# Optimization experiments

Measured on AMD Instinct MI355X. Metric: run time of the kernel, lower is better.

The kernel has to match this reference:

```python
import jax, jax.numpy as jnp
import numpy as np

B, R, H, W = 8, 128, 4096, 4096

def setup_inputs() -> dict:
    key = jax.random.key(0)
    k1, k2, k3, k4 = jax.random.split(key, 4)
    N = jax.random.normal(k1, (B, 1, R, W), dtype=jnp.float32)
    Ak_L = jax.random.normal(k2, (B, 1, H, W), dtype=jnp.float32)
    alpha = jax.random.uniform(k3, (B,), dtype=jnp.float32)
    gamma = jax.random.uniform(k4, (B,), dtype=jnp.float32)
    return {"N": N, "Ak_L": Ak_L, "alpha": alpha, "gamma": gamma}

def reference(N, Ak_L, alpha, gamma):
    # N: [B,1,r,W], Ak_L: [B,1,H,W], alpha/gamma: [B]
    b = N.shape[0]
    r = N.shape[2]
    a = alpha.reshape(b, 1, 1, 1)
    g = gamma.reshape(b, 1, 1, 1)
    I = jnp.eye(r, dtype=N.dtype)  # broadcast over [B,1,r,r]
    # C = alpha*I + 2*gamma * N @ N^T  -> [B,1,r,r]
    C = a * I + 2.0 * g * jnp.einsum('bcrw,bcsw->bcrs', N, N)
    Cinv = jnp.linalg.pinv(C)  # batched pinv over [B,1]
    # X = (Ak_L @ N^T) @ pinv(C) -> [B,1,H,r]
    AN = jnp.einsum('bchw,bcrw->bchr', Ak_L, N)
    X = jnp.einsum('bchr,bcrs->bchs', AN, Cinv)
    return 2.0 * g * X
```

## Files before the change

### kernel.cpp

```cpp
#include <hip/hip_runtime.h>


typedef __attribute__((ext_vector_type(8))) short bf16x8;
typedef __attribute__((ext_vector_type(4))) float f32x4;
typedef __attribute__((ext_vector_type(4))) unsigned int u32x4;

#define MFMA16(a, b, c) __builtin_amdgcn_mfma_f32_16x16x32_bf16((a), (b), (c), 0, 0, 0)

__device__ __forceinline__ unsigned short f2bf(float f) {
  union { float f; unsigned u; } v; v.f = f;
  unsigned u = v.u;
  return (unsigned short)((u + 0x7FFFu + ((u >> 16) & 1u)) >> 16);
}
__device__ __forceinline__ unsigned pack2(float x, float y) {
  return (unsigned)f2bf(x) | ((unsigned)f2bf(y) << 16);
}

__global__ __launch_bounds__(256) void k_castT(const float* __restrict__ N,
                                               unsigned short* __restrict__ NT) {
  __attribute__((aligned(16))) __shared__ float tile[128 * 68];
  int wc = blockIdx.x, b = blockIdx.y;
  const float* Nb = N + (size_t)b * 524288 + wc * 64;
  int t = threadIdx.x;
  int row = t >> 1, half = t & 1;
  const float* src = Nb + (size_t)row * 4096 + half * 32;
  float* dst = tile + row * 68 + half * 32;
#pragma unroll
  for (int j = 0; j < 8; j++) *(f32x4*)(dst + j * 4) = *(const f32x4*)(src + j * 4);
  __syncthreads();
  int ow = t >> 2, q = t & 3;
  unsigned short* out = NT + (size_t)b * 524288 + (size_t)(wc * 64 + ow) * 128 + q * 32;
#pragma unroll
  for (int c = 0; c < 4; c++) {
    u32x4 p;
#pragma unroll
    for (int k = 0; k < 4; k++) {
      float f0 = tile[(q * 32 + c * 8 + k * 2) * 68 + ow];
      float f1 = tile[(q * 32 + c * 8 + k * 2 + 1) * 68 + ow];
      p[k] = pack2(f0, f1);
    }
    *(u32x4*)(out + c * 8) = p;
  }
}

__global__ __launch_bounds__(256) void k_gram(const float* __restrict__ N,
                                              float* __restrict__ Gpart) {
  __attribute__((aligned(16))) __shared__ unsigned short lds[128 * 72];
  int ks = blockIdx.x, b = blockIdx.y;
  const float* Nb = N + (size_t)b * 524288 + ks * 1024;
  int t = threadIdx.x;
  int wave = t >> 6, lane = t & 63, quad = lane >> 4, l16 = lane & 15;
  f32x4 acc[2][8];
#pragma unroll
  for (int i = 0; i < 2; i++)
#pragma unroll
    for (int j = 0; j < 8; j++) acc[i][j] = (f32x4){0.f, 0.f, 0.f, 0.f};
  int srow = t >> 1, shalf = t & 1;
  const float* srcb = Nb + (size_t)srow * 4096 + shalf * 32;
  unsigned short* dptr = lds + srow * 72 + shalf * 32;
  for (int it = 0; it < 16; ++it) {
    u32x4 pk0, pk1;
    {
      f32x4 v0 = *(const f32x4*)(srcb + it * 64 + 0);
      f32x4 v1 = *(const f32x4*)(srcb + it * 64 + 4);
      f32x4 v2 = *(const f32x4*)(srcb + it * 64 + 8);
      f32x4 v3 = *(const f32x4*)(srcb + it * 64 + 12);
      pk0[0] = pack2(v0[0], v0[1]); pk0[1] = pack2(v0[2], v0[3]);
      pk0[2] = pack2(v1[0], v1[1]); pk0[3] = pack2(v1[2], v1[3]);
      pk1[0] = pack2(v2[0], v2[1]); pk1[1] = pack2(v2[2], v2[3]);
      pk1[2] = pack2(v3[0], v3[1]); pk1[3] = pack2(v3[2], v3[3]);
    }
    u32x4 pk2, pk3;
    {
      f32x4 v0 = *(const f32x4*)(srcb + it * 64 + 16);
      f32x4 v1 = *(const f32x4*)(srcb + it * 64 + 20);
      f32x4 v2 = *(const f32x4*)(srcb + it * 64 + 24);
      f32x4 v3 = *(const f32x4*)(srcb + it * 64 + 28);
      pk2[0] = pack2(v0[0], v0[1]); pk2[1] = pack2(v0[2], v0[3]);
      pk2[2] = pack2(v1[0], v1[1]); pk2[3] = pack2(v1[2], v1[3]);
      pk3[0] = pack2(v2[0], v2[1]); pk3[1] = pack2(v2[2], v2[3]);
      pk3[2] = pack2(v3[0], v3[1]); pk3[3] = pack2(v3[2], v3[3]);
    }
    __syncthreads();
    *(u32x4*)(dptr + 0) = pk0;
    *(u32x4*)(dptr + 8) = pk1;
    *(u32x4*)(dptr + 16) = pk2;
    *(u32x4*)(dptr + 24) = pk3;
    __syncthreads();
    bf16x8 af[2][2], bfv[8][2];
#pragma unroll
    for (int mt = 0; mt < 2; mt++)
#pragma unroll
      for (int kk = 0; kk < 2; kk++)
        af[mt][kk] = *(const bf16x8*)(lds + (wave * 32 + mt * 16 + l16) * 72 + (kk * 4 + quad) * 8);
#pragma unroll
    for (int nt = 0; nt < 8; nt++)
#pragma unroll
      for (int kk = 0; kk < 2; kk++)
        bfv[nt][kk] = *(const bf16x8*)(lds + (nt * 16 + l16) * 72 + (kk * 4 + quad) * 8);
#pragma unroll
    for (int mt = 0; mt < 2; mt++)
#pragma unroll
      for (int nt = 0; nt < 8; nt++)
#pragma unroll
        for (int kk = 0; kk < 2; kk++)
          acc[mt][nt] = MFMA16(af[mt][kk], bfv[nt][kk], acc[mt][nt]);
  }
  float* Gp = Gpart + ((size_t)(b * 4 + ks) << 14);
#pragma unroll
  for (int mt = 0; mt < 2; mt++)
#pragma unroll
    for (int nt = 0; nt < 8; nt++)
#pragma unroll
      for (int rg = 0; rg < 4; rg++) {
        int row = wave * 32 + mt * 16 + quad * 4 + rg;
        int col = nt * 16 + l16;
        Gp[row * 128 + col] = acc[mt][nt][rg];
      }
}

__global__ __launch_bounds__(1024) void k_inv(const float* __restrict__ Gpart,
                                              const float* __restrict__ alpha,
                                              const float* __restrict__ gamma,
                                              float* __restrict__ Cinv) {
  __attribute__((aligned(16))) __shared__ float Cs[16384];
  __attribute__((aligned(16))) __shared__ float mcol[2][128];
  __attribute__((aligned(16))) __shared__ float pivrow[2][256];
  int b = blockIdx.x;
  int t = threadIdx.x;
  const float* Gp = Gpart + ((size_t)b * 4 << 14);
#pragma unroll
  for (int c = 0; c < 4; c++) {
    int off = c * 4096 + t * 4;
    f32x4 v0 = *(const f32x4*)(Gp + off);
    f32x4 v1 = *(const f32x4*)(Gp + 16384 + off);
    f32x4 v2 = *(const f32x4*)(Gp + 32768 + off);
    f32x4 v3 = *(const f32x4*)(Gp + 49152 + off);
    *(f32x4*)(Cs + off) = v0 + v1 + v2 + v3;
  }
  __syncthreads();
  int rb = t & 31, cg = t >> 5;
  float al = alpha[b], ga2 = 2.f * gamma[b];
  float a[4][8];
#pragma unroll
  for (int i = 0; i < 4; i++) {
    int r = rb * 4 + i;
#pragma unroll
    for (int j = 0; j < 8; j++) {
      if (cg < 16) {
        int c = cg * 8 + j;
        a[i][j] = ga2 * Cs[r * 128 + c] + ((r == c) ? al : 0.f);
      } else {
        int c = (cg - 16) * 8 + j;
        a[i][j] = (r == c) ? 1.f : 0.f;
      }
    }
  }
  __syncthreads();
  for (int p = 0; p < 128; ++p) {
    int pb = p & 1;
    int cgp = p >> 3, jp = p & 7, rbp = p >> 2, ip = p & 3;
    if (cg == cgp) {
      float m0, m1, m2, m3;
      switch (jp) {
        case 0: m0 = a[0][0]; m1 = a[1][0]; m2 = a[2][0]; m3 = a[3][0]; break;
        case 1: m0 = a[0][1]; m1 = a[1][1]; m2 = a[2][1]; m3 = a[3][1]; break;
        case 2: m0 = a[0][2]; m1 = a[1][2]; m2 = a[2][2]; m3 = a[3][2]; break;
        case 3: m0 = a[0][3]; m1 = a[1][3]; m2 = a[2][3]; m3 = a[3][3]; break;
        case 4: m0 = a[0][4]; m1 = a[1][4]; m2 = a[2][4]; m3 = a[3][4]; break;
        case 5: m0 = a[0][5]; m1 = a[1][5]; m2 = a[2][5]; m3 = a[3][5]; break;
        case 6: m0 = a[0][6]; m1 = a[1][6]; m2 = a[2][6]; m3 = a[3][6]; break;
        default: m0 = a[0][7]; m1 = a[1][7]; m2 = a[2][7]; m3 = a[3][7]; break;
      }
      *(f32x4*)&mcol[pb][rb * 4] = (f32x4){m0, m1, m2, m3};
    }
    __syncthreads();
    if (rb == rbp) {
      float d = mcol[pb][p];
      float invd = 1.0f / d;
      switch (ip) {
        case 0: {
#pragma unroll
          for (int j = 0; j < 8; j++) a[0][j] *= invd;
          *(f32x4*)&pivrow[pb][cg * 8] = (f32x4){a[0][0], a[0][1], a[0][2], a[0][3]};
          *(f32x4*)&pivrow[pb][cg * 8 + 4] = (f32x4){a[0][4], a[0][5], a[0][6], a[0][7]};
        } break;
        case 1: {
#pragma unroll
          for (int j = 0; j < 8; j++) a[1][j] *= invd;
          *(f32x4*)&pivrow[pb][cg * 8] = (f32x4){a[1][0], a[1][1], a[1][2], a[1][3]};
          *(f32x4*)&pivrow[pb][cg * 8 + 4] = (f32x4){a[1][4], a[1][5], a[1][6], a[1][7]};
        } break;
        case 2: {
#pragma unroll
          for (int j = 0; j < 8; j++) a[2][j] *= invd;
          *(f32x4*)&pivrow[pb][cg * 8] = (f32x4){a[2][0], a[2][1], a[2][2], a[2][3]};
          *(f32x4*)&pivrow[pb][cg * 8 + 4] = (f32x4){a[2][4], a[2][5], a[2][6], a[2][7]};
        } break;
        default: {
#pragma unroll
          for (int j = 0; j < 8; j++) a[3][j] *= invd;
          *(f32x4*)&pivrow[pb][cg * 8] = (f32x4){a[3][0], a[3][1], a[3][2], a[3][3]};
          *(f32x4*)&pivrow[pb][cg * 8 + 4] = (f32x4){a[3][4], a[3][5], a[3][6], a[3][7]};
        } break;
      }
    }
    __syncthreads();
    f32x4 mc = *(const f32x4*)&mcol[pb][rb * 4];
    f32x4 p0 = *(const f32x4*)&pivrow[pb][cg * 8];
    f32x4 p1 = *(const f32x4*)&pivrow[pb][cg * 8 + 4];
#pragma unroll
    for (int i = 0; i < 4; i++) {
      int r = rb * 4 + i;
      float m = (r == p) ? 0.f : mc[i];
#pragma unroll
      for (int j = 0; j < 4; j++) a[i][j] -= m * p0[j];
#pragma unroll
      for (int j = 0; j < 4; j++) a[i][4 + j] -= m * p1[j];
    }
  }
  if (cg >= 16) {
    float* dst = Cinv + ((size_t)b << 14);
    int c0 = (cg - 16) * 8;
#pragma unroll
    for (int i = 0; i < 4; i++) {
      int r = rb * 4 + i;
      *(f32x4*)(dst + r * 128 + c0) = (f32x4){a[i][0], a[i][1], a[i][2], a[i][3]};
      *(f32x4*)(dst + r * 128 + c0 + 4) = (f32x4){a[i][4], a[i][5], a[i][6], a[i][7]};
    }
  }
}

__global__ __launch_bounds__(256) void k_mt(const float* __restrict__ Cinv,
                                            const unsigned short* __restrict__ NT,
                                            const float* __restrict__ gamma,
                                            unsigned short* __restrict__ Mt) {
  __attribute__((aligned(16))) __shared__ unsigned short la[128 * 72];
  __attribute__((aligned(16))) __shared__ unsigned short lb[128 * 72];
  int wc = blockIdx.x, b = blockIdx.y;
  int w0 = wc * 128;
  float ga2 = 2.f * gamma[b];
  const float* Cb = Cinv + ((size_t)b << 14);
  const unsigned short* NTb = NT + (size_t)b * 524288;
  int t = threadIdx.x, wave = t >> 6, lane = t & 63, quad = lane >> 4, l16 = lane & 15;
  f32x4 acc[2][8];
#pragma unroll
  for (int i = 0; i < 2; i++)
#pragma unroll
    for (int j = 0; j < 8; j++) acc[i][j] = (f32x4){0.f, 0.f, 0.f, 0.f};
  int row = t >> 1, half = t & 1;
  const float* asrc = Cb + (size_t)row * 128 + half * 32;
  const unsigned short* bsrc = NTb + (size_t)(w0 + row) * 128 + half * 32;
  unsigned short* adst = la + row * 72 + half * 32;
  unsigned short* bdst = lb + row * 72 + half * 32;
  for (int it = 0; it < 2; ++it) {
    int k0 = it * 64;
    u32x4 pa0, pa1;
    {
      f32x4 v0 = *(const f32x4*)(asrc + k0 + 0);
      f32x4 v1 = *(const f32x4*)(asrc + k0 + 4);
      f32x4 v2 = *(const f32x4*)(asrc + k0 + 8);
      f32x4 v3 = *(const f32x4*)(asrc + k0 + 12);
      pa0[0] = pack2(ga2 * v0[0], ga2 * v0[1]); pa0[1] = pack2(ga2 * v0[2], ga2 * v0[3]);
      pa0[2] = pack2(ga2 * v1[0], ga2 * v1[1]); pa0[3] = pack2(ga2 * v1[2], ga2 * v1[3]);
      pa1[0] = pack2(ga2 * v2[0], ga2 * v2[1]); pa1[1] = pack2(ga2 * v2[2], ga2 * v2[3]);
      pa1[2] = pack2(ga2 * v3[0], ga2 * v3[1]); pa1[3] = pack2(ga2 * v3[2], ga2 * v3[3]);
    }
    u32x4 pa2, pa3;
    {
      f32x4 v0 = *(const f32x4*)(asrc + k0 + 16);
      f32x4 v1 = *(const f32x4*)(asrc + k0 + 20);
      f32x4 v2 = *(const f32x4*)(asrc + k0 + 24);
      f32x4 v3 = *(const f32x4*)(asrc + k0 + 28);
      pa2[0] = pack2(ga2 * v0[0], ga2 * v0[1]); pa2[1] = pack2(ga2 * v0[2], ga2 * v0[3]);
      pa2[2] = pack2(ga2 * v1[0], ga2 * v1[1]); pa2[3] = pack2(ga2 * v1[2], ga2 * v1[3]);
      pa3[0] = pack2(ga2 * v2[0], ga2 * v2[1]); pa3[1] = pack2(ga2 * v2[2], ga2 * v2[3]);
      pa3[2] = pack2(ga2 * v3[0], ga2 * v3[1]); pa3[3] = pack2(ga2 * v3[2], ga2 * v3[3]);
    }
    u32x4 bv0 = *(const u32x4*)(bsrc + k0 + 0);
    u32x4 bv1 = *(const u32x4*)(bsrc + k0 + 8);
    u32x4 bv2 = *(const u32x4*)(bsrc + k0 + 16);
    u32x4 bv3 = *(const u32x4*)(bsrc + k0 + 24);
    __syncthreads();
    *(u32x4*)(adst + 0) = pa0;  *(u32x4*)(adst + 8) = pa1;
    *(u32x4*)(adst + 16) = pa2; *(u32x4*)(adst + 24) = pa3;
    *(u32x4*)(bdst + 0) = bv0;  *(u32x4*)(bdst + 8) = bv1;
    *(u32x4*)(bdst + 16) = bv2; *(u32x4*)(bdst + 24) = bv3;
    __syncthreads();
    bf16x8 af[2][2], bfv[8][2];
#pragma unroll
    for (int mt = 0; mt < 2; mt++)
#pragma unroll
      for (int kk = 0; kk < 2; kk++)
        af[mt][kk] = *(const bf16x8*)(la + (wave * 32 + mt * 16 + l16) * 72 + (kk * 4 + quad) * 8);
#pragma unroll
    for (int nt = 0; nt < 8; nt++)
#pragma unroll
      for (int kk = 0; kk < 2; kk++)
        bfv[nt][kk] = *(const bf16x8*)(lb + (nt * 16 + l16) * 72 + (kk * 4 + quad) * 8);
#pragma unroll
    for (int mt = 0; mt < 2; mt++)
#pragma unroll
      for (int nt = 0; nt < 8; nt++)
#pragma unroll
        for (int kk = 0; kk < 2; kk++)
          acc[mt][nt] = MFMA16(af[mt][kk], bfv[nt][kk], acc[mt][nt]);
    __syncthreads();
  }
  unsigned short* Mb = Mt + (size_t)b * 524288;
#pragma unroll
  for (int mt = 0; mt < 2; mt++)
#pragma unroll
    for (int nt = 0; nt < 8; nt++)
#pragma unroll
      for (int rg = 0; rg < 4; rg++) {
        int r = wave * 32 + mt * 16 + quad * 4 + rg;
        int w = w0 + nt * 16 + l16;
        Mb[(size_t)r * 4096 + w] = f2bf(acc[mt][nt][rg]);
      }
}

__global__ __launch_bounds__(256) void k_gemm(const float* __restrict__ A,
                                              const unsigned short* __restrict__ Mt,
                                              float* __restrict__ out) {
  __attribute__((aligned(16))) __shared__ unsigned short la[64 * 72];
  __attribute__((aligned(16))) __shared__ unsigned short lb[128 * 72];
  int mtile = blockIdx.x, b = blockIdx.y;
  const float* Ab = A + (size_t)b * 16777216 + (size_t)mtile * 64 * 4096;
  const unsigned short* Mb = Mt + (size_t)b * 524288;
  int t = threadIdx.x, wave = t >> 6, lane = t & 63, quad = lane >> 4, l16 = lane & 15;
  int wm = wave >> 1, wr = wave & 1;
  f32x4 acc[2][4];
#pragma unroll
  for (int i = 0; i < 2; i++)
#pragma unroll
    for (int j = 0; j < 4; j++) acc[i][j] = (f32x4){0.f, 0.f, 0.f, 0.f};
  int arow = t >> 2, aq = t & 3;
  int brow = t >> 1, bhalf = t & 1;
  const float* asrc = Ab + (size_t)arow * 4096 + aq * 16;
  const unsigned short* bsrc = Mb + (size_t)brow * 4096 + bhalf * 32;
  unsigned short* adst = la + arow * 72 + aq * 16;
  unsigned short* bdst = lb + brow * 72 + bhalf * 32;
  for (int it = 0; it < 64; ++it) {
    int k0 = it * 64;
    f32x4 av0 = *(const f32x4*)(asrc + k0 + 0);
    f32x4 av1 = *(const f32x4*)(asrc + k0 + 4);
    f32x4 av2 = *(const f32x4*)(asrc + k0 + 8);
    f32x4 av3 = *(const f32x4*)(asrc + k0 + 12);
    u32x4 bv0 = *(const u32x4*)(bsrc + k0 + 0);
    u32x4 bv1 = *(const u32x4*)(bsrc + k0 + 8);
    u32x4 bv2 = *(const u32x4*)(bsrc + k0 + 16);
    u32x4 bv3 = *(const u32x4*)(bsrc + k0 + 24);
    u32x4 pa0, pa1;
    pa0[0] = pack2(av0[0], av0[1]); pa0[1] = pack2(av0[2], av0[3]);
    pa0[2] = pack2(av1[0], av1[1]); pa0[3] = pack2(av1[2], av1[3]);
    pa1[0] = pack2(av2[0], av2[1]); pa1[1] = pack2(av2[2], av2[3]);
    pa1[2] = pack2(av3[0], av3[1]); pa1[3] = pack2(av3[2], av3[3]);
    __syncthreads();
    *(u32x4*)(adst + 0) = pa0;
    *(u32x4*)(adst + 8) = pa1;
    *(u32x4*)(bdst + 0) = bv0;
    *(u32x4*)(bdst + 8) = bv1;
    *(u32x4*)(bdst + 16) = bv2;
    *(u32x4*)(bdst + 24) = bv3;
    __syncthreads();
    bf16x8 af[2][2], bfv[4][2];
#pragma unroll
    for (int mt = 0; mt < 2; mt++)
#pragma unroll
      for (int kk = 0; kk < 2; kk++)
        af[mt][kk] = *(const bf16x8*)(la + (wm * 32 + mt * 16 + l16) * 72 + (kk * 4 + quad) * 8);
#pragma unroll
    for (int rt = 0; rt < 4; rt++)
#pragma unroll
      for (int kk = 0; kk < 2; kk++)
        bfv[rt][kk] = *(const bf16x8*)(lb + (wr * 64 + rt * 16 + l16) * 72 + (kk * 4 + quad) * 8);
#pragma unroll
    for (int mt = 0; mt < 2; mt++)
#pragma unroll
      for (int rt = 0; rt < 4; rt++)
#pragma unroll
        for (int kk = 0; kk < 2; kk++)
          acc[mt][rt] = MFMA16(af[mt][kk], bfv[rt][kk], acc[mt][rt]);
  }
  float* ob = out + (size_t)b * 524288 + (size_t)mtile * 64 * 128;
#pragma unroll
  for (int mt = 0; mt < 2; mt++)
#pragma unroll
    for (int rt = 0; rt < 4; rt++)
#pragma unroll
      for (int rg = 0; rg < 4; rg++) {
        int h = wm * 32 + mt * 16 + quad * 4 + rg;
        int r = wr * 64 + rt * 16 + l16;
        ob[h * 128 + r] = acc[mt][rt][rg];
      }
}

extern "C" void kernel_launch(void* const* d_in, const int* in_sizes, int n_in,
                              void* d_out, int out_size, void* d_ws, size_t ws_size,
                              hipStream_t stream) {
  const float* N = (const float*)d_in[0];
  const float* Ak = (const float*)d_in[1];
  const float* alpha = (const float*)d_in[2];
  const float* gamma = (const float*)d_in[3];
  float* out = (float*)d_out;
  char* ws = (char*)d_ws;
  unsigned short* NT = (unsigned short*)(ws);
  float* Gpart = (float*)(ws + 8388608);
  float* Cinv = (float*)(ws + 10485760);
  unsigned short* Mt = (unsigned short*)(ws + 11010048);

  k_castT<<<dim3(64, 8), 256, 0, stream>>>(N, NT);
  k_gram<<<dim3(4, 8), 256, 0, stream>>>(N, Gpart);
  k_inv<<<dim3(8), 1024, 0, stream>>>(Gpart, alpha, gamma, Cinv);
  k_mt<<<dim3(32, 8), 256, 0, stream>>>(Cinv, NT, gamma, Mt);
  k_gemm<<<dim3(64, 8), 256, 0, stream>>>(Ak, Mt, out);
}
```

Before: 889.0 us.

## Split Gram reduction wider, in-place Gauss-Jordan inverse, prefetch GEMM loads, interleave batches

The Gram kernel now splits K eight ways instead of four, giving more blocks to fill the GPU, and the inverse kernel sums eight partials. The inverse switches from an augmented [C|I] Gauss-Jordan to an in-place variant where each thread holds a 4x4 tile, which halves register state and removes one barrier per pivot. The GEMM register-prefetches the next K tile's global loads across the compute step, and its grid is flattened with batch as the fastest index. These changes add a larger partial buffer and shift workspace offsets, and the in-place inversion is unpivoted like before.

```diff
diff --git a/kernel.cpp b/kernel.cpp
--- a/kernel.cpp
+++ b/kernel.cpp
@@ -6,6 +6,7 @@
 typedef __attribute__((ext_vector_type(4))) unsigned int u32x4;
 
 #define MFMA16(a, b, c) __builtin_amdgcn_mfma_f32_16x16x32_bf16((a), (b), (c), 0, 0, 0)
+#define NSPLIT 8
 
 __device__ __forceinline__ unsigned short f2bf(float f) {
   union { float f; unsigned u; } v; v.f = f;
@@ -47,7 +48,7 @@
                                               float* __restrict__ Gpart) {
   __attribute__((aligned(16))) __shared__ unsigned short lds[128 * 72];
   int ks = blockIdx.x, b = blockIdx.y;
-  const float* Nb = N + (size_t)b * 524288 + ks * 1024;
+  const float* Nb = N + (size_t)b * 524288 + ks * 512;
   int t = threadIdx.x;
   int wave = t >> 6, lane = t & 63, quad = lane >> 4, l16 = lane & 15;
   f32x4 acc[2][8];
@@ -58,7 +59,7 @@
   int srow = t >> 1, shalf = t & 1;
   const float* srcb = Nb + (size_t)srow * 4096 + shalf * 32;
   unsigned short* dptr = lds + srow * 72 + shalf * 32;
-  for (int it = 0; it < 16; ++it) {
+  for (int it = 0; it < 8; ++it) {
     u32x4 pk0, pk1;
     {
       f32x4 v0 = *(const f32x4*)(srcb + it * 64 + 0);
@@ -106,7 +107,7 @@
         for (int kk = 0; kk < 2; kk++)
           acc[mt][nt] = MFMA16(af[mt][kk], bfv[nt][kk], acc[mt][nt]);
   }
-  float* Gp = Gpart + ((size_t)(b * 4 + ks) << 14);
+  float* Gp = Gpart + ((size_t)(b * NSPLIT + ks) << 14);
 #pragma unroll
   for (int mt = 0; mt < 2; mt++)
 #pragma unroll
@@ -125,109 +126,74 @@
                                               float* __restrict__ Cinv) {
   __attribute__((aligned(16))) __shared__ float Cs[16384];
   __attribute__((aligned(16))) __shared__ float mcol[2][128];
-  __attribute__((aligned(16))) __shared__ float pivrow[2][256];
+  __attribute__((aligned(16))) __shared__ float pivrow[2][128];
   int b = blockIdx.x;
   int t = threadIdx.x;
-  const float* Gp = Gpart + ((size_t)b * 4 << 14);
+  const float* Gp = Gpart + ((size_t)b * NSPLIT << 14);
 #pragma unroll
   for (int c = 0; c < 4; c++) {
     int off = c * 4096 + t * 4;
-    f32x4 v0 = *(const f32x4*)(Gp + off);
-    f32x4 v1 = *(const f32x4*)(Gp + 16384 + off);
-    f32x4 v2 = *(const f32x4*)(Gp + 32768 + off);
-    f32x4 v3 = *(const f32x4*)(Gp + 49152 + off);
-    *(f32x4*)(Cs + off) = v0 + v1 + v2 + v3;
+    f32x4 s = (f32x4){0.f, 0.f, 0.f, 0.f};
+#pragma unroll
+    for (int ks = 0; ks < NSPLIT; ks++) s += *(const f32x4*)(Gp + ks * 16384 + off);
+    *(f32x4*)(Cs + off) = s;
   }
   __syncthreads();
-  int rb = t & 31, cg = t >> 5;
+  int cg = t & 31, rb = t >> 5;
   float al = alpha[b], ga2 = 2.f * gamma[b];
-  float a[4][8];
+  float a[4][4];
 #pragma unroll
   for (int i = 0; i < 4; i++) {
     int r = rb * 4 + i;
-#pragma unroll
-    for (int j = 0; j < 8; j++) {
-      if (cg < 16) {
-        int c = cg * 8 + j;
-        a[i][j] = ga2 * Cs[r * 128 + c] + ((r == c) ? al : 0.f);
-      } else {
-        int c = (cg - 16) * 8 + j;
-        a[i][j] = (r == c) ? 1.f : 0.f;
-      }
-    }
-  }
-  __syncthreads();
+    f32x4 v = *(const f32x4*)(Cs + r * 128 + cg * 4);
+#pragma unroll
+    for (int j = 0; j < 4; j++) {
+      int c = cg * 4 + j;
+      a[i][j] = ga2 * v[j] + ((r == c) ? al : 0.f);
+    }
+  }
   for (int p = 0; p < 128; ++p) {
     int pb = p & 1;
-    int cgp = p >> 3, jp = p & 7, rbp = p >> 2, ip = p & 3;
+    int cgp = p >> 2, jp = p & 3;
+    int rbp = p >> 2, ip = p & 3;
     if (cg == cgp) {
-      float m0, m1, m2, m3;
-      switch (jp) {
-        case 0: m0 = a[0][0]; m1 = a[1][0]; m2 = a[2][0]; m3 = a[3][0]; break;
-        case 1: m0 = a[0][1]; m1 = a[1][1]; m2 = a[2][1]; m3 = a[3][1]; break;
-        case 2: m0 = a[0][2]; m1 = a[1][2]; m2 = a[2][2]; m3 = a[3][2]; break;
-        case 3: m0 = a[0][3]; m1 = a[1][3]; m2 = a[2][3]; m3 = a[3][3]; break;
-        case 4: m0 = a[0][4]; m1 = a[1][4]; m2 = a[2][4]; m3 = a[3][4]; break;
-        case 5: m0 = a[0][5]; m1 = a[1][5]; m2 = a[2][5]; m3 = a[3][5]; break;
-        case 6: m0 = a[0][6]; m1 = a[1][6]; m2 = a[2][6]; m3 = a[3][6]; break;
-        default: m0 = a[0][7]; m1 = a[1][7]; m2 = a[2][7]; m3 = a[3][7]; break;
-      }
-      *(f32x4*)&mcol[pb][rb * 4] = (f32x4){m0, m1, m2, m3};
-    }
-    __syncthreads();
+      f32x4 mv;
+#pragma unroll
+      for (int i = 0; i < 4; i++)
+        mv[i] = (jp & 2) ? ((jp & 1) ? a[i][3] : a[i][2]) : ((jp & 1) ? a[i][1] : a[i][0]);
+      *(f32x4*)&mcol[pb][rb * 4] = mv;
+    }
     if (rb == rbp) {
-      float d = mcol[pb][p];
-      float invd = 1.0f / d;
-      switch (ip) {
-        case 0: {
-#pragma unroll
-          for (int j = 0; j < 8; j++) a[0][j] *= invd;
-          *(f32x4*)&pivrow[pb][cg * 8] = (f32x4){a[0][0], a[0][1], a[0][2], a[0][3]};
-          *(f32x4*)&pivrow[pb][cg * 8 + 4] = (f32x4){a[0][4], a[0][5], a[0][6], a[0][7]};
-        } break;
-        case 1: {
-#pragma unroll
-          for (int j = 0; j < 8; j++) a[1][j] *= invd;
-          *(f32x4*)&pivrow[pb][cg * 8] = (f32x4){a[1][0], a[1][1], a[1][2], a[1][3]};
-          *(f32x4*)&pivrow[pb][cg * 8 + 4] = (f32x4){a[1][4], a[1][5], a[1][6], a[1][7]};
-        } break;
-        case 2: {
-#pragma unroll
-          for (int j = 0; j < 8; j++) a[2][j] *= invd;
-          *(f32x4*)&pivrow[pb][cg * 8] = (f32x4){a[2][0], a[2][1], a[2][2], a[2][3]};
-          *(f32x4*)&pivrow[pb][cg * 8 + 4] = (f32x4){a[2][4], a[2][5], a[2][6], a[2][7]};
-        } break;
-        default: {
-#pragma unroll
-          for (int j = 0; j < 8; j++) a[3][j] *= invd;
-          *(f32x4*)&pivrow[pb][cg * 8] = (f32x4){a[3][0], a[3][1], a[3][2], a[3][3]};
-          *(f32x4*)&pivrow[pb][cg * 8 + 4] = (f32x4){a[3][4], a[3][5], a[3][6], a[3][7]};
-        } break;
-      }
-    }
-    __syncthreads();
+      f32x4 pv;
+#pragma unroll
+      for (int j = 0; j < 4; j++)
+        pv[j] = (ip & 2) ? ((ip & 1) ? a[3][j] : a[2][j]) : ((ip & 1) ? a[1][j] : a[0][j]);
+      *(f32x4*)&pivrow[pb][cg * 4] = pv;
+    }
+    __syncthreads();
+    float invd = 1.0f / mcol[pb][p];
     f32x4 mc = *(const f32x4*)&mcol[pb][rb * 4];
-    f32x4 p0 = *(const f32x4*)&pivrow[pb][cg * 8];
-    f32x4 p1 = *(const f32x4*)&pivrow[pb][cg * 8 + 4];
+    f32x4 pr = *(const f32x4*)&pivrow[pb][cg * 4];
 #pragma unroll
     for (int i = 0; i < 4; i++) {
       int r = rb * 4 + i;
-      float m = (r == p) ? 0.f : mc[i];
-#pragma unroll
-      for (int j = 0; j < 4; j++) a[i][j] -= m * p0[j];
-#pragma unroll
-      for (int j = 0; j < 4; j++) a[i][4 + j] -= m * p1[j];
-    }
-  }
-  if (cg >= 16) {
-    float* dst = Cinv + ((size_t)b << 14);
-    int c0 = (cg - 16) * 8;
-#pragma unroll
-    for (int i = 0; i < 4; i++) {
-      int r = rb * 4 + i;
-      *(f32x4*)(dst + r * 128 + c0) = (f32x4){a[i][0], a[i][1], a[i][2], a[i][3]};
-      *(f32x4*)(dst + r * 128 + c0 + 4) = (f32x4){a[i][4], a[i][5], a[i][6], a[i][7]};
-    }
+      float mi = mc[i] * invd;
+#pragma unroll
+      for (int j = 0; j < 4; j++) {
+        int c = cg * 4 + j;
+        float v = a[i][j] - mi * pr[j];
+        if (c == p) v = -mi;
+        if (r == p) v = pr[j] * invd;
+        if (r == p && c == p) v = invd;
+        a[i][j] = v;
+      }
+    }
+  }
+  float* dst = Cinv + ((size_t)b << 14);
+#pragma unroll
+  for (int i = 0; i < 4; i++) {
+    int r = rb * 4 + i;
+    *(f32x4*)(dst + r * 128 + cg * 4) = (f32x4){a[i][0], a[i][1], a[i][2], a[i][3]};
   }
 }
 
@@ -325,7 +291,8 @@
                                               float* __restrict__ out) {
   __attribute__((aligned(16))) __shared__ unsigned short la[64 * 72];
   __attribute__((aligned(16))) __shared__ unsigned short lb[128 * 72];
-  int mtile = blockIdx.x, b = blockIdx.y;
+  int blk = blockIdx.x;
+  int b = blk & 7, mtile = blk >> 3;
   const float* Ab = A + (size_t)b * 16777216 + (size_t)mtile * 64 * 4096;
   const unsigned short* Mb = Mt + (size_t)b * 524288;
   int t = threadIdx.x, wave = t >> 6, lane = t & 63, quad = lane >> 4, l16 = lane & 15;
@@ -341,16 +308,15 @@
   const unsigned short* bsrc = Mb + (size_t)brow * 4096 + bhalf * 32;
   unsigned short* adst = la + arow * 72 + aq * 16;
   unsigned short* bdst = lb + brow * 72 + bhalf * 32;
+  f32x4 av0 = *(const f32x4*)(asrc + 0);
+  f32x4 av1 = *(const f32x4*)(asrc + 4);
+  f32x4 av2 = *(const f32x4*)(asrc + 8);
+  f32x4 av3 = *(const f32x4*)(asrc + 12);
+  u32x4 bv0 = *(const u32x4*)(bsrc + 0);
+  u32x4 bv1 = *(const u32x4*)(bsrc + 8);
+  u32x4 bv2 = *(const u32x4*)(bsrc + 16);
+  u32x4 bv3 = *(const u32x4*)(bsrc + 24);
   for (int it = 0; it < 64; ++it) {
-    int k0 = it * 64;
-    f32x4 av0 = *(const f32x4*)(asrc + k0 + 0);
-    f32x4 av1 = *(const f32x4*)(asrc + k0 + 4);
-    f32x4 av2 = *(const f32x4*)(asrc + k0 + 8);
-    f32x4 av3 = *(const f32x4*)(asrc + k0 + 12);
-    u32x4 bv0 = *(const u32x4*)(bsrc + k0 + 0);
-    u32x4 bv1 = *(const u32x4*)(bsrc + k0 + 8);
-    u32x4 bv2 = *(const u32x4*)(bsrc + k0 + 16);
-    u32x4 bv3 = *(const u32x4*)(bsrc + k0 + 24);
     u32x4 pa0, pa1;
     pa0[0] = pack2(av0[0], av0[1]); pa0[1] = pack2(av0[2], av0[3]);
     pa0[2] = pack2(av1[0], av1[1]); pa0[3] = pack2(av1[2], av1[3]);
@@ -364,6 +330,17 @@
     *(u32x4*)(bdst + 16) = bv2;
     *(u32x4*)(bdst + 24) = bv3;
     __syncthreads();
+    if (it < 63) {
+      int k0 = (it + 1) * 64;
+      av0 = *(const f32x4*)(asrc + k0 + 0);
+      av1 = *(const f32x4*)(asrc + k0 + 4);
+      av2 = *(const f32x4*)(asrc + k0 + 8);
+      av3 = *(const f32x4*)(asrc + k0 + 12);
+      bv0 = *(const u32x4*)(bsrc + k0 + 0);
+      bv1 = *(const u32x4*)(bsrc + k0 + 8);
+      bv2 = *(const u32x4*)(bsrc + k0 + 16);
+      bv3 = *(const u32x4*)(bsrc + k0 + 24);
+    }
     bf16x8 af[2][2], bfv[4][2];
 #pragma unroll
     for (int mt = 0; mt < 2; mt++)
@@ -407,12 +384,12 @@
   char* ws = (char*)d_ws;
   unsigned short* NT = (unsigned short*)(ws);
   float* Gpart = (float*)(ws + 8388608);
-  float* Cinv = (float*)(ws + 10485760);
-  unsigned short* Mt = (unsigned short*)(ws + 11010048);
+  float* Cinv = (float*)(ws + 12582912);
+  unsigned short* Mt = (unsigned short*)(ws + 13107200);
 
   k_castT<<<dim3(64, 8), 256, 0, stream>>>(N, NT);
-  k_gram<<<dim3(4, 8), 256, 0, stream>>>(N, Gpart);
+  k_gram<<<dim3(NSPLIT, 8), 256, 0, stream>>>(N, Gpart);
   k_inv<<<dim3(8), 1024, 0, stream>>>(Gpart, alpha, gamma, Cinv);
   k_mt<<<dim3(32, 8), 256, 0, stream>>>(Cinv, NT, gamma, Mt);
-  k_gemm<<<dim3(64, 8), 256, 0, stream>>>(Ak, Mt, out);
-}
+  k_gemm<<<dim3(512), 256, 0, stream>>>(Ak, Mt, out);
+}
```

Measured after the change: 858.9 us. -3.4%, faster.
